# Kernel optimization log

Measured on AMD Instinct MI355X. Metric: run time of the kernel, lower is better.

The kernel has to match this reference:

```python
import jax, jax.numpy as jnp
import numpy as np

DIM = 1024        # BIGNET_DIM
GS = 16           # group_size
N_LAYERS = 18     # 6 blocks * 3 QLoRALinear
N_BLOCKS = 6
R = 32            # lora_dim
B = 32768         # flattened batch/tokens
LN_EPS = 1e-5


def _qlora_linear(x, qw, sc, b, la, lb):
    # Dequantize int4 weights: per-group (group_size=16 along in_features) scale.
    O, I = qw.shape
    w = (qw.astype(jnp.float32).reshape(O, I // GS, GS) * sc[:, :, None]).reshape(O, I)
    base = x @ w.T + b                      # [B, O] dequant-matmul
    lora = (x @ la.T) @ lb.T                # fp32 low-rank branch [B,R]->[B,O]
    return base + lora


def _layernorm(x, g, b):
    mu = jnp.mean(x, axis=-1, keepdims=True)
    var = jnp.mean((x - mu) ** 2, axis=-1, keepdims=True)
    return (x - mu) * jax.lax.rsqrt(var + LN_EPS) * g + b


def setup_inputs() -> dict:
    key = jax.random.key(0)
    ks = jax.random.split(key, 6)
    x = jax.random.normal(ks[0], (B, DIM), dtype=jnp.float32)
    # int4 codes in [-8, 7]
    qw = jax.random.randint(ks[1], (N_LAYERS, DIM, DIM), -8, 8, dtype=jnp.int32)
    # positive per-group scales (absmax/7-like magnitude)
    scales = jax.random.uniform(ks[2], (N_LAYERS, DIM, DIM // GS), dtype=jnp.float32,
                                minval=0.005, maxval=0.02)
    bias = 0.02 * jax.random.normal(ks[3], (N_LAYERS, DIM), dtype=jnp.float32)
    lora_a = (1.0 / np.sqrt(DIM)) * jax.random.normal(ks[4], (N_LAYERS, R, DIM), dtype=jnp.float32)
    # lora_b is zero-init in the module; use small random values so the branch is exercised
    lora_b = 0.01 * jax.random.normal(ks[5], (N_LAYERS, DIM, R), dtype=jnp.float32)
    ln_g = jnp.ones((N_BLOCKS - 1, DIM), dtype=jnp.float32)
    ln_b = jnp.zeros((N_BLOCKS - 1, DIM), dtype=jnp.float32)
    return {"x": x, "qw": qw, "scales": scales, "bias": bias,
            "lora_a": lora_a, "lora_b": lora_b, "ln_g": ln_g, "ln_b": ln_b}


def reference(x, qw, scales, bias, lora_a, lora_b, ln_g, ln_b):
    h = x
    for blk in range(N_BLOCKS):
        y = h
        for j in range(3):
            li = blk * 3 + j
            y = _qlora_linear(y, qw[li], scales[li], bias[li], lora_a[li], lora_b[li])
            if j < 2:
                y = jax.nn.relu(y)
        h = y + h                     # residual
        if blk < N_BLOCKS - 1:
            h = _layernorm(h, ln_g[blk], ln_b[blk])
    return h
```

## Files before the change

kernel.cpp:

```cpp
#include <hip/hip_runtime.h>
#include <cstdint>

typedef _Float16 f16;
typedef _Float16 f16x8 __attribute__((ext_vector_type(8)));
typedef _Float16 f16x4 __attribute__((ext_vector_type(4)));
typedef float    f32x4 __attribute__((ext_vector_type(4)));

#define DIMN 1024
#define BATCH 32768
#define NLAYERS 18
#define NBLOCKS 6

__device__ __forceinline__ void gl2lds16(const f16* g, const f16* l) {
    auto gp = (const __attribute__((address_space(1))) unsigned int*)(uintptr_t)g;
    auto lp = (__attribute__((address_space(3))) unsigned int*)(uintptr_t)l;
    __builtin_amdgcn_global_load_lds(gp, lp, 16, 0, 0);
}

__global__ void cvt_kernel(const float* __restrict__ x, f16* __restrict__ o) {
    int i = (blockIdx.x * 256 + threadIdx.x) * 4;
    float4 v = *(const float4*)&x[i];
    f16x4 r;
    r[0] = (f16)v.x; r[1] = (f16)v.y; r[2] = (f16)v.z; r[3] = (f16)v.w;
    *(f16x4*)&o[i] = r;
}

__global__ __launch_bounds__(256) void prep_w_kernel(
        const int* __restrict__ qw, const float* __restrict__ sc,
        const float* __restrict__ la, const float* __restrict__ lb,
        f16* __restrict__ W) {
    int b = blockIdx.x;
    int li = b >> 7;
    int og = (b & 127) << 3;
    __shared__ float lbs[8][32];
    int tid = threadIdx.x;
    lbs[tid >> 5][tid & 31] = lb[((size_t)li * 1024 + og + (tid >> 5)) * 32 + (tid & 31)];
    __syncthreads();

    int i0 = tid * 4;
    const float* laL = la + (size_t)li * 32 * 1024;
    float acc[8][4] = {};
    for (int r = 0; r < 32; ++r) {
        float4 lav = *(const float4*)&laL[r * 1024 + i0];
#pragma unroll
        for (int q = 0; q < 8; ++q) {
            float wv = lbs[q][r];
            acc[q][0] += wv * lav.x; acc[q][1] += wv * lav.y;
            acc[q][2] += wv * lav.z; acc[q][3] += wv * lav.w;
        }
    }
#pragma unroll
    for (int q = 0; q < 8; ++q) {
        size_t row = (size_t)li * 1024 + og + q;
        size_t rowbase = row * 1024;
        int4 code = *(const int4*)&qw[rowbase + i0];
        float scale = sc[row * 64 + (i0 >> 4)];
        f16x4 o;
        o[0] = (f16)((float)code.x * scale + acc[q][0]);
        o[1] = (f16)((float)code.y * scale + acc[q][1]);
        o[2] = (f16)((float)code.z * scale + acc[q][2]);
        o[3] = (f16)((float)code.w * scale + acc[q][3]);
        *(f16x4*)&W[rowbase + i0] = o;
    }
}

#define LDC 136
__global__ __launch_bounds__(256, 3) void gemm_kernel(
        const f16* __restrict__ A, const f16* __restrict__ W,
        const float* __restrict__ bias, f16* __restrict__ C, int relu) {
    __shared__ __align__(16) char smem[128 * LDC * 2];
    f16* As = (f16*)smem;
    f16* Bs = (f16*)(smem + 8192);
    f16* Cs = (f16*)smem;

    int tid = threadIdx.x;
    int l = tid & 63, w = tid >> 6;
    int wm = w & 1, wn = w >> 1;

    int bid = blockIdx.x;
    int mg = bid >> 6;
    int inner = bid & 63;
    int mt = (mg << 3) | (inner & 7);
    int nt = (inner >> 3) & 7;
    int bm = mt * 128, bn = nt * 128;

    int row0 = tid >> 2, kc0 = tid & 3;
    const f16* a0 = A + (size_t)(bm + row0) * DIMN + kc0 * 8;
    const f16* a1 = a0 + (size_t)64 * DIMN;
    const f16* b0 = W + (size_t)(bn + row0) * DIMN + kc0 * 8;
    const f16* b1 = b0 + (size_t)64 * DIMN;
    f16* lA0 = As + w * 512;
    f16* lA1 = As + 2048 + w * 512;
    f16* lB0 = Bs + w * 512;
    f16* lB1 = Bs + 2048 + w * 512;

    f32x4 acc[4][4] = {};

    int mrow = wm * 64 + (l & 15);
    int nrow = wn * 64 + (l & 15);
    int q8 = (l >> 4) * 8;

    for (int kt = 0; kt < DIMN; kt += 32) {
        gl2lds16(a0 + kt, lA0);
        gl2lds16(a1 + kt, lA1);
        gl2lds16(b0 + kt, lB0);
        gl2lds16(b1 + kt, lB1);
        asm volatile("s_waitcnt vmcnt(0)" ::: "memory");
        __syncthreads();

        f16x8 af[4], bfr[4];
#pragma unroll
        for (int i = 0; i < 4; ++i) {
            af[i]  = *(const f16x8*)&As[(mrow + i * 16) * 32 + q8];
            bfr[i] = *(const f16x8*)&Bs[(nrow + i * 16) * 32 + q8];
        }
#pragma unroll
        for (int i = 0; i < 4; ++i)
#pragma unroll
            for (int j = 0; j < 4; ++j)
                acc[i][j] = __builtin_amdgcn_mfma_f32_16x16x32_f16(
                    af[i], bfr[j], acc[i][j], 0, 0, 0);
        __syncthreads();
    }

    int col0 = wn * 64 + (l & 15);
    int rloc = wm * 64 + (l >> 4) * 4;
    float bsv[4];
#pragma unroll
    for (int j = 0; j < 4; ++j) bsv[j] = bias[bn + col0 + j * 16];
#pragma unroll
    for (int i = 0; i < 4; ++i)
#pragma unroll
        for (int j = 0; j < 4; ++j)
#pragma unroll
            for (int r = 0; r < 4; ++r) {
                float v = acc[i][j][r] + bsv[j];
                if (relu) v = fmaxf(v, 0.f);
                Cs[(rloc + i * 16 + r) * LDC + col0 + j * 16] = (f16)v;
            }
    __syncthreads();
    int c8 = (tid & 15) * 8;
    int r0 = tid >> 4;
#pragma unroll
    for (int it = 0; it < 8; ++it) {
        int row = r0 + it * 16;
        f16x8 val = *(const f16x8*)&Cs[row * LDC + c8];
        *(f16x8*)&C[(size_t)(bm + row) * DIMN + bn + c8] = val;
    }
}

__global__ void res_ln_kernel(const f16* __restrict__ y, f16* __restrict__ h,
                              const float* __restrict__ g, const float* __restrict__ b,
                              float* __restrict__ outF, int mode) {
    int row = blockIdx.x;
    int tid = threadIdx.x;
    int c0 = tid * 4;
    const f16* yr = y + (size_t)row * DIMN;
    f16* hr = h + (size_t)row * DIMN;

    f16x4 yv = *(const f16x4*)&yr[c0];
    f16x4 hv = *(const f16x4*)&hr[c0];
    float v[4];
    float s = 0.f, sq = 0.f;
#pragma unroll
    for (int i = 0; i < 4; ++i) {
        v[i] = (float)yv[i] + (float)hv[i];
        s += v[i]; sq += v[i] * v[i];
    }
#pragma unroll
    for (int o = 32; o > 0; o >>= 1) {
        s += __shfl_xor(s, o);
        sq += __shfl_xor(sq, o);
    }
    __shared__ float red[8];
    int wv = tid >> 6, ln = tid & 63;
    if (ln == 0) { red[wv] = s; red[4 + wv] = sq; }
    __syncthreads();
    float S1 = red[0] + red[1] + red[2] + red[3];
    float S2 = red[4] + red[5] + red[6] + red[7];
    float mu = S1 * (1.f / 1024.f);
    float var = S2 * (1.f / 1024.f) - mu * mu;
    float rs = rsqrtf(var + 1e-5f);

    if (mode == 0) {
        float4 gv = *(const float4*)&g[c0];
        float4 bv = *(const float4*)&b[c0];
        f16x4 outv;
        outv[0] = (f16)((v[0] - mu) * rs * gv.x + bv.x);
        outv[1] = (f16)((v[1] - mu) * rs * gv.y + bv.y);
        outv[2] = (f16)((v[2] - mu) * rs * gv.z + bv.z);
        outv[3] = (f16)((v[3] - mu) * rs * gv.w + bv.w);
        *(f16x4*)&hr[c0] = outv;
    } else {
        float4 ov;
        ov.x = v[0]; ov.y = v[1]; ov.z = v[2]; ov.w = v[3];
        *(float4*)&outF[(size_t)row * DIMN + c0] = ov;
    }
}

extern "C" void kernel_launch(void* const* d_in, const int* in_sizes, int n_in,
                              void* d_out, int out_size, void* d_ws, size_t ws_size,
                              hipStream_t stream) {
    const float* x    = (const float*)d_in[0];
    const int*   qw   = (const int*)d_in[1];
    const float* sc   = (const float*)d_in[2];
    const float* bias = (const float*)d_in[3];
    const float* la   = (const float*)d_in[4];
    const float* lb   = (const float*)d_in[5];
    const float* lng  = (const float*)d_in[6];
    const float* lnb  = (const float*)d_in[7];
    float* out = (float*)d_out;

    char* ws = (char*)d_ws;
    f16* Weff = (f16*)ws;
    f16* H    = (f16*)(ws + (size_t)37748736);
    f16* P    = (f16*)(ws + (size_t)37748736 + 67108864);
    f16* Q    = (f16*)d_out;

    cvt_kernel<<<BATCH * DIMN / (256 * 4), 256, 0, stream>>>(x, H);
    prep_w_kernel<<<NLAYERS * 128, 256, 0, stream>>>(qw, sc, la, lb, Weff);

    for (int blk = 0; blk < NBLOCKS; ++blk) {
        for (int j = 0; j < 3; ++j) {
            int li = blk * 3 + j;
            const f16* in = (j == 0) ? H : ((j == 1) ? P : Q);
            f16* o = (j == 1) ? Q : P;
            gemm_kernel<<<2048, 256, 0, stream>>>(
                in, Weff + ((size_t)li << 20), bias + li * 1024, o, (j < 2) ? 1 : 0);
        }
        int lnidx = (blk < 5) ? blk : 4;
        res_ln_kernel<<<BATCH, 256, 0, stream>>>(
            P, H, lng + lnidx * 1024, lnb + lnidx * 1024, out, (blk == 5) ? 1 : 0);
    }
}
```

Before: 1.918 ms.

## Rewrite GEMM with 256x256 tiles, 4-stage LDS pipeline and swizzled layout

The GEMM kernel now uses 512-thread blocks computing 256x256 output tiles, with a four-buffer global-to-LDS prefetch pipeline so loads for upcoming K-slices overlap the MFMA work on the current one. LDS rows are XOR-swizzled to avoid bank conflicts, the block-to-tile mapping groups tiles per XCD for L2 reuse, and s_setprio raises priority around the MFMA burst. The aim is to cut memory stalls and the per-iteration barrier cost of the old single-buffered 128x128 kernel. In exchange it uses 128KB of LDS and more accumulator registers per thread, which lowers occupancy, and the grid shrinks to 512 blocks.

After: 1.859 ms. 1.03x faster.

```diff
diff --git a/kernel.cpp b/kernel.cpp
--- a/kernel.cpp
+++ b/kernel.cpp
@@ -64,88 +64,109 @@
     }
 }
 
-#define LDC 136
-__global__ __launch_bounds__(256, 3) void gemm_kernel(
+__global__ __launch_bounds__(512, 2) void gemm_kernel(
         const f16* __restrict__ A, const f16* __restrict__ W,
         const float* __restrict__ bias, f16* __restrict__ C, int relu) {
-    __shared__ __align__(16) char smem[128 * LDC * 2];
-    f16* As = (f16*)smem;
-    f16* Bs = (f16*)(smem + 8192);
-    f16* Cs = (f16*)smem;
+    __shared__ __align__(16) char smem[131072];
 
     int tid = threadIdx.x;
     int l = tid & 63, w = tid >> 6;
-    int wm = w & 1, wn = w >> 1;
-
-    int bid = blockIdx.x;
-    int mg = bid >> 6;
-    int inner = bid & 63;
-    int mt = (mg << 3) | (inner & 7);
-    int nt = (inner >> 3) & 7;
-    int bm = mt * 128, bn = nt * 128;
-
-    int row0 = tid >> 2, kc0 = tid & 3;
-    const f16* a0 = A + (size_t)(bm + row0) * DIMN + kc0 * 8;
-    const f16* a1 = a0 + (size_t)64 * DIMN;
-    const f16* b0 = W + (size_t)(bn + row0) * DIMN + kc0 * 8;
-    const f16* b1 = b0 + (size_t)64 * DIMN;
-    f16* lA0 = As + w * 512;
-    f16* lA1 = As + 2048 + w * 512;
-    f16* lB0 = Bs + w * 512;
-    f16* lB1 = Bs + 2048 + w * 512;
-
-    f32x4 acc[4][4] = {};
-
-    int mrow = wm * 64 + (l & 15);
-    int nrow = wn * 64 + (l & 15);
-    int q8 = (l >> 4) * 8;
-
-    for (int kt = 0; kt < DIMN; kt += 32) {
-        gl2lds16(a0 + kt, lA0);
-        gl2lds16(a1 + kt, lA1);
-        gl2lds16(b0 + kt, lB0);
-        gl2lds16(b1 + kt, lB1);
-        asm volatile("s_waitcnt vmcnt(0)" ::: "memory");
+    int wm = w >> 2, wn = w & 3;
+
+    int hb = blockIdx.x;
+    int xcd = hb & 7, idx = hb >> 3;
+    int mt = xcd * 16 + (idx >> 2);
+    int nt = idx & 3;
+    int bm = mt * 256, bn = nt * 256;
+
+    int ss = ((tid & 3) ^ ((tid >> 3) & 3)) * 8;
+    const f16* Ag0 = A + (size_t)(bm + (tid >> 2)) * DIMN + ss;
+    const f16* Ag1 = Ag0 + (size_t)128 * DIMN;
+    const f16* Bg0 = W + (size_t)(bn + (tid >> 2)) * DIMN + ss;
+    const f16* Bg1 = Bg0 + (size_t)128 * DIMN;
+    int ldst = tid * 16;
+
+    int lr = l & 15;
+    int slot = ((l >> 4) ^ (lr >> 1)) & 3;
+    int byteA = (wm * 128 + lr) * 64 + slot * 16;
+    int byteB = (wn * 64 + lr) * 64 + slot * 16 + 16384;
+
+    f32x4 acc[8][4] = {};
+
+#pragma unroll
+    for (int p = 0; p < 3; ++p) {
+        char* bse = smem + p * 32768;
+        gl2lds16(Ag0 + p * 32, (const f16*)(bse + ldst));
+        gl2lds16(Ag1 + p * 32, (const f16*)(bse + 8192 + ldst));
+        gl2lds16(Bg0 + p * 32, (const f16*)(bse + 16384 + ldst));
+        gl2lds16(Bg1 + p * 32, (const f16*)(bse + 24576 + ldst));
+    }
+    asm volatile("s_waitcnt vmcnt(8)" ::: "memory");
+    __builtin_amdgcn_s_barrier();
+    asm volatile("" ::: "memory");
+
+    for (int kt = 0; kt < 32; ++kt) {
+        int kp = (kt + 3) & 31;
+        char* bse = smem + ((kt + 3) & 3) * 32768;
+        gl2lds16(Ag0 + kp * 32, (const f16*)(bse + ldst));
+        gl2lds16(Ag1 + kp * 32, (const f16*)(bse + 8192 + ldst));
+        gl2lds16(Bg0 + kp * 32, (const f16*)(bse + 16384 + ldst));
+        gl2lds16(Bg1 + kp * 32, (const f16*)(bse + 24576 + ldst));
+
+        const char* buf = smem + (kt & 3) * 32768;
+        f16x8 af[8], bf[4];
+#pragma unroll
+        for (int m = 0; m < 8; ++m)
+            af[m] = *(const f16x8*)(buf + byteA + m * 1024);
+#pragma unroll
+        for (int n = 0; n < 4; ++n)
+            bf[n] = *(const f16x8*)(buf + byteB + n * 1024);
+
+        __builtin_amdgcn_s_setprio(1);
+#pragma unroll
+        for (int m = 0; m < 8; ++m)
+#pragma unroll
+            for (int n = 0; n < 4; ++n)
+                acc[m][n] = __builtin_amdgcn_mfma_f32_16x16x32_f16(
+                    af[m], bf[n], acc[m][n], 0, 0, 0);
+        __builtin_amdgcn_s_setprio(0);
+
+        asm volatile("s_waitcnt vmcnt(8)" ::: "memory");
+        __builtin_amdgcn_s_barrier();
+        asm volatile("" ::: "memory");
+    }
+
+    __syncthreads();
+    f16* Cs = (f16*)smem;
+    const int LDC2 = 264;
+    int gc = wn * 64 + lr;
+    float bsv[4];
+#pragma unroll
+    for (int j = 0; j < 4; ++j) bsv[j] = bias[bn + gc + j * 16];
+    int r0 = (l >> 4) * 4;
+    int srow = tid >> 5, sc8 = (tid & 31) * 8;
+#pragma unroll
+    for (int half = 0; half < 2; ++half) {
+        if (wm == half) {
+#pragma unroll
+            for (int m = 0; m < 8; ++m)
+#pragma unroll
+                for (int j = 0; j < 4; ++j)
+#pragma unroll
+                    for (int r = 0; r < 4; ++r) {
+                        float v = acc[m][j][r] + bsv[j];
+                        if (relu) v = fmaxf(v, 0.f);
+                        Cs[(m * 16 + r0 + r) * LDC2 + gc + j * 16] = (f16)v;
+                    }
+        }
         __syncthreads();
-
-        f16x8 af[4], bfr[4];
-#pragma unroll
-        for (int i = 0; i < 4; ++i) {
-            af[i]  = *(const f16x8*)&As[(mrow + i * 16) * 32 + q8];
-            bfr[i] = *(const f16x8*)&Bs[(nrow + i * 16) * 32 + q8];
-        }
-#pragma unroll
-        for (int i = 0; i < 4; ++i)
-#pragma unroll
-            for (int j = 0; j < 4; ++j)
-                acc[i][j] = __builtin_amdgcn_mfma_f32_16x16x32_f16(
-                    af[i], bfr[j], acc[i][j], 0, 0, 0);
-        __syncthreads();
-    }
-
-    int col0 = wn * 64 + (l & 15);
-    int rloc = wm * 64 + (l >> 4) * 4;
-    float bsv[4];
-#pragma unroll
-    for (int j = 0; j < 4; ++j) bsv[j] = bias[bn + col0 + j * 16];
-#pragma unroll
-    for (int i = 0; i < 4; ++i)
-#pragma unroll
-        for (int j = 0; j < 4; ++j)
-#pragma unroll
-            for (int r = 0; r < 4; ++r) {
-                float v = acc[i][j][r] + bsv[j];
-                if (relu) v = fmaxf(v, 0.f);
-                Cs[(rloc + i * 16 + r) * LDC + col0 + j * 16] = (f16)v;
-            }
-    __syncthreads();
-    int c8 = (tid & 15) * 8;
-    int r0 = tid >> 4;
-#pragma unroll
-    for (int it = 0; it < 8; ++it) {
-        int row = r0 + it * 16;
-        f16x8 val = *(const f16x8*)&Cs[row * LDC + c8];
-        *(f16x8*)&C[(size_t)(bm + row) * DIMN + bn + c8] = val;
+#pragma unroll
+        for (int it = 0; it < 8; ++it) {
+            int row = srow + it * 16;
+            f16x8 val = *(const f16x8*)&Cs[row * LDC2 + sc8];
+            *(f16x8*)&C[(size_t)(bm + half * 128 + row) * DIMN + bn + sc8] = val;
+        }
+        if (half == 0) __syncthreads();
     }
 }
 
@@ -225,7 +246,7 @@
             int li = blk * 3 + j;
             const f16* in = (j == 0) ? H : ((j == 1) ? P : Q);
             f16* o = (j == 1) ? Q : P;
-            gemm_kernel<<<2048, 256, 0, stream>>>(
+            gemm_kernel<<<512, 512, 0, stream>>>(
                 in, Weff + ((size_t)li << 20), bias + li * 1024, o, (j < 2) ? 1 : 0);
         }
         int lnidx = (blk < 5) ? blk : 4;
```
